# Optimization experiments

Measured on AMD Instinct MI355X. Metric: run time of the kernel, lower is better.

## Reference

```python
import jax, jax.numpy as jnp
import numpy as np

EPS = 1e-12  # torch F.normalize eps

def setup_inputs() -> dict:
    key = jax.random.key(0)
    ks = jax.random.split(key, 3)
    B, N, C, H, K = 4, 4096, 512, 8, 64
    x = jax.random.normal(ks[0], (B, N, C), dtype=jnp.float32)
    W_qkvv = jax.random.normal(ks[1], (4 * C, C), dtype=jnp.float32) * (1.0 / np.sqrt(C))
    # init_: uniform(-1/sqrt(K), 1/sqrt(K)) over [N, K]
    std = 1.0 / np.sqrt(K)
    EF = jax.random.uniform(ks[2], (N, K), dtype=jnp.float32, minval=-std, maxval=std)
    temperature = jnp.ones((H, 1, 1), dtype=jnp.float32)
    temperature2 = jnp.ones((H, 1, 1), dtype=jnp.float32)
    return {"x": x, "W_qkvv": W_qkvv, "EF": EF,
            "temperature": temperature, "temperature2": temperature2}

def _l2norm(t):
    # torch.nn.functional.normalize(dim=-1): x / max(||x||_2, eps)
    n = jnp.sqrt(jnp.sum(t * t, axis=-1, keepdims=True))
    return t / jnp.maximum(n, EPS)

def reference(x, W_qkvv, EF, temperature, temperature2):
    B, N, C = x.shape
    H = temperature.shape[0]
    d = C // H
    # fused QKVV projection (no bias)
    qkvv = (x @ W_qkvv.T).reshape(B, N, 4, H, d)
    qkvv = jnp.transpose(qkvv, (2, 0, 3, 1, 4))  # [4,B,H,N,d]
    # transpose last two dims -> [B,H,d,N]
    q = jnp.swapaxes(qkvv[0], -2, -1)
    k = jnp.swapaxes(qkvv[1], -2, -1)
    v_CA = jnp.swapaxes(qkvv[2], -2, -1)
    v_SA = jnp.swapaxes(qkvv[3], -2, -1)
    # Linformer-style EF projection over token axis: [B,H,d,N] x [N,K] -> [B,H,d,K]
    k_proj = jnp.einsum('bhdn,nk->bhdk', k, EF)
    v_proj = jnp.einsum('bhdn,nk->bhdk', v_SA, EF)
    # L2-normalize q,k over token axis
    qn = _l2norm(q)
    kn = _l2norm(k)
    # channel attention: [B,H,d,d]
    attn_CA = jax.nn.softmax(jnp.einsum('bhdn,bhen->bhde', qn, kn) * temperature, axis=-1)
    x_CA = jnp.einsum('bhde,bhen->bhdn', attn_CA, v_CA)           # [B,H,d,N]
    x_CA = jnp.transpose(x_CA, (0, 3, 1, 2)).reshape(B, N, C)      # [B,N,C]
    # spatial attention via projected K: [B,H,N,K]
    attn_SA = jax.nn.softmax(jnp.einsum('bhdn,bhdk->bhnk', qn, k_proj) * temperature2, axis=-1)
    x_SA = jnp.einsum('bhnk,bhdk->bhnd', attn_SA, v_proj)          # [B,H,N,d]
    # faithful to the original: permute(0,3,1,2) then reshape(B,N,C)
    x_SA = jnp.transpose(x_SA, (0, 3, 1, 2)).reshape(B, N, C)
    return x_CA + x_SA
```

## Files before the change

### kernel.cpp

```cpp
#include <hip/hip_runtime.h>

typedef unsigned short u16;
typedef unsigned int u32;
typedef __attribute__((ext_vector_type(8))) short s16x8;
typedef __attribute__((ext_vector_type(4))) float f32x4;

#define MFMA16(a,b,c) __builtin_amdgcn_mfma_f32_16x16x32_bf16(a,b,c,0,0,0)

__device__ __forceinline__ u16 f2bf(float f){
  u32 u = __builtin_bit_cast(u32, f);
  return (u16)((u + 0x7FFFu + ((u >> 16) & 1u)) >> 16);
}
__device__ __forceinline__ float b2f(u16 s){
  u32 u = ((u32)s) << 16;
  return __builtin_bit_cast(float, u);
}
__device__ __forceinline__ int sw64(int row, int col){
  return row * 64 + ((((col >> 3) ^ row) & 7) << 3) + (col & 7);
}
__device__ __forceinline__ void async16(const void* g, void* l){
  __builtin_amdgcn_global_load_lds((const __attribute__((address_space(1))) u32*)g,
                                   (__attribute__((address_space(3))) u32*)l, 16, 0, 0);
}


__global__ __launch_bounds__(256) void k_convert(const float4* __restrict__ x4,
                                                 const float4* __restrict__ w4,
                                                 const float* __restrict__ EF,
                                                 u16* __restrict__ Xb, u16* __restrict__ Wb,
                                                 u16* __restrict__ EFt){
  int i = blockIdx.x * 256 + threadIdx.x;
  if (i < 2097152){
    float4 v = x4[i];
    u32 lo = (u32)f2bf(v.x) | ((u32)f2bf(v.y) << 16);
    u32 hi = (u32)f2bf(v.z) | ((u32)f2bf(v.w) << 16);
    *(uint2*)(&Xb[(size_t)i*4]) = make_uint2(lo, hi);
  } else if (i < 2097152 + 262144){
    int j = i - 2097152;
    float4 v = w4[j];
    u32 lo = (u32)f2bf(v.x) | ((u32)f2bf(v.y) << 16);
    u32 hi = (u32)f2bf(v.z) | ((u32)f2bf(v.w) << 16);
    *(uint2*)(&Wb[(size_t)j*4]) = make_uint2(lo, hi);
  } else if (i < 2097152 + 262144 + 262144){
    int j = i - 2097152 - 262144;
    int kk = j >> 12, nn = j & 4095;
    EFt[(size_t)kk*4096 + nn] = f2bf(EF[(size_t)nn*64 + kk]);
  }
}

__global__ __launch_bounds__(256) void k_gemm(const u16* __restrict__ Wb,
                                              const u16* __restrict__ Xb,
                                              u16* __restrict__ Out){
  __shared__ u16 smA[128*32];
  __shared__ u16 smB[128*32];
  int bid = blockIdx.x;
  int ot = bid & 15, mt = bid >> 4;
  int o0 = ot * 128, m0 = mt * 128;
  int t = threadIdx.x;
  int lane = t & 63, w = t >> 6;
  int wr = w >> 1, wc = w & 1;
  int l15 = lane & 15, l4 = lane >> 4;
  f32x4 acc[4][4];
#pragma unroll
  for (int a = 0; a < 4; ++a)
#pragma unroll
    for (int b = 0; b < 4; ++b) acc[a][b] = (f32x4){0.f, 0.f, 0.f, 0.f};

  for (int kt = 0; kt < 16; ++kt){
    int kb = kt * 32;
#pragma unroll
    for (int i = 0; i < 2; ++i){
      int la = t + 256 * i;
      async16(Wb + (size_t)(o0 + (la >> 2)) * 512 + kb + (la & 3) * 8, &smA[la * 8]);
      async16(Xb + (size_t)(m0 + (la >> 2)) * 512 + kb + (la & 3) * 8, &smB[la * 8]);
    }
    __syncthreads();
    s16x8 af[4], bfr[4];
#pragma unroll
    for (int rf = 0; rf < 4; ++rf) af[rf] = *(const s16x8*)(&smA[(wr*64 + rf*16 + l15)*32 + l4*8]);
#pragma unroll
    for (int cf = 0; cf < 4; ++cf) bfr[cf] = *(const s16x8*)(&smB[(wc*64 + cf*16 + l15)*32 + l4*8]);
#pragma unroll
    for (int rf = 0; rf < 4; ++rf)
#pragma unroll
      for (int cf = 0; cf < 4; ++cf)
        acc[rf][cf] = MFMA16(af[rf], bfr[cf], acc[rf][cf]);
    __syncthreads();
  }
#pragma unroll
  for (int rf = 0; rf < 4; ++rf)
#pragma unroll
    for (int cf = 0; cf < 4; ++cf){
      int o = o0 + wr*64 + rf*16 + l4*4;
      int m = m0 + wc*64 + cf*16 + l15;
#pragma unroll
      for (int r = 0; r < 4; ++r) Out[(size_t)(o + r) * 16384 + m] = f2bf(acc[rf][cf][r]);
    }
}

__global__ __launch_bounds__(64) void k_rnorm(const u16* __restrict__ QK,
                                              float* __restrict__ rq, float* __restrict__ rk){
  int bid = blockIdx.x;
  int o = bid >> 2, b = bid & 3;
  int lane = threadIdx.x;
  const u16* row = QK + (size_t)o * 16384 + (size_t)b * 4096;
  float s = 0.f;
#pragma unroll
  for (int it = 0; it < 8; ++it){
    s16x8 v = *(const s16x8*)(&row[it * 512 + lane * 8]);
#pragma unroll
    for (int j = 0; j < 8; ++j){ float f = b2f((u16)v[j]); s += f * f; }
  }
  for (int off = 32; off; off >>= 1) s += __shfl_down(s, off);
  if (lane == 0){
    float r = 1.f / fmaxf(sqrtf(s), 1e-12f);
    if (o < 512) rq[b * 512 + o] = r;
    else         rk[b * 512 + (o - 512)] = r;
  }
}

__global__ __launch_bounds__(256) void k_acc1(const u16* __restrict__ QK,
                                              const u16* __restrict__ EFt,
                                              float* __restrict__ Pp){
  int bid = blockIdx.x;
  int p = bid >> 8;
  int rem = bid & 255;
  int bh = rem >> 3, s = rem & 7;
  int b = bh >> 3, h = bh & 7;
  int t = threadIdx.x, lane = t & 63, w = t >> 6, l15 = lane & 15, l4 = lane >> 4;
  int abase = (p == 0 ? 0 : (p == 1 ? 512 : 1536)) + h * 64;
  const u16* aptr = QK + (size_t)(abase + w*16 + l15) * 16384 + (size_t)b * 4096 + s * 512;
  f32x4 acc[4];
#pragma unroll
  for (int c = 0; c < 4; ++c) acc[c] = (f32x4){0.f,0.f,0.f,0.f};

  if (p == 0){
    const u16* bptr = QK + (size_t)(512 + h*64 + l15) * 16384 + (size_t)b * 4096 + s * 512;
#pragma unroll 2
    for (int ks = 0; ks < 16; ++ks){
      int n = ks * 32 + l4 * 8;
      s16x8 a = *(const s16x8*)(aptr + n);
#pragma unroll
      for (int cf = 0; cf < 4; ++cf){
        s16x8 bb = *(const s16x8*)(bptr + (size_t)cf * 16 * 16384 + n);
        acc[cf] = MFMA16(a, bb, acc[cf]);
      }
    }
  } else {
    const u16* bptr = EFt + (size_t)l15 * 4096 + s * 512;
#pragma unroll 2
    for (int ks = 0; ks < 16; ++ks){
      int n = ks * 32 + l4 * 8;
      s16x8 a = *(const s16x8*)(aptr + n);
#pragma unroll
      for (int cf = 0; cf < 4; ++cf){
        s16x8 bb = *(const s16x8*)(bptr + (size_t)cf * 16 * 4096 + n);
        acc[cf] = MFMA16(a, bb, acc[cf]);
      }
    }
  }

  float* out = Pp + ((size_t)(bh * 3 + p) * 8 + s) * 4096;
#pragma unroll
  for (int cf = 0; cf < 4; ++cf)
#pragma unroll
    for (int r = 0; r < 4; ++r){
      int rr = w*16 + l4*4 + r;
      int cc = cf*16 + l15;
      int off = (p == 1) ? (cc * 64 + rr) : (rr * 64 + cc);
      out[off] = acc[cf][r];
    }
}

__global__ __launch_bounds__(256) void k_fin(const float* __restrict__ Pp,
                                             const float* __restrict__ rq,
                                             const float* __restrict__ rk,
                                             const float* __restrict__ t1,
                                             const float* __restrict__ t2,
                                             u16* __restrict__ Pca,
                                             u16* __restrict__ kpb,
                                             u16* __restrict__ vpb){
  int bh = blockIdx.x;
  int b = bh >> 3, h = bh & 7;
  int t = threadIdx.x;
  int row = t >> 2, q4 = t & 3;
  const float* base = Pp + (size_t)bh * 3 * 8 * 4096;
  float t1h = t1[h], t2h = t2[h];
  const float* rqh = rq + b*512 + h*64;
  const float* rkh = rk + b*512 + h*64;

  {
    float v[16];
#pragma unroll
    for (int i = 0; i < 4; ++i){
      f32x4 a = (f32x4){0.f,0.f,0.f,0.f};
#pragma unroll
      for (int s = 0; s < 8; ++s)
        a += *(const f32x4*)(base + (size_t)s * 4096 + t*16 + i*4);
#pragma unroll
      for (int j = 0; j < 4; ++j) v[i*4 + j] = a[j];
    }
    float sq = rqh[row] * t1h;
#pragma unroll
    for (int e = 0; e < 16; ++e) v[e] *= sq * rkh[q4*16 + e];
    float mx = v[0];
#pragma unroll
    for (int e = 1; e < 16; ++e) mx = fmaxf(mx, v[e]);
    mx = fmaxf(mx, __shfl_xor(mx, 1));
    mx = fmaxf(mx, __shfl_xor(mx, 2));
    float sum = 0.f;
#pragma unroll
    for (int e = 0; e < 16; ++e){ v[e] = __expf(v[e] - mx); sum += v[e]; }
    sum += __shfl_xor(sum, 1);
    sum += __shfl_xor(sum, 2);
    float inv = 1.f / sum;
    s16x8 o0, o1;
#pragma unroll
    for (int e = 0; e < 8; ++e){ o0[e] = (short)f2bf(v[e] * inv); o1[e] = (short)f2bf(v[8+e] * inv); }
    *(s16x8*)(&Pca[(size_t)bh*4096 + t*16])     = o0;
    *(s16x8*)(&Pca[(size_t)bh*4096 + t*16 + 8]) = o1;
  }
  {
    const float* p1 = base + 8 * 4096;
    float v[16];
#pragma unroll
    for (int i = 0; i < 4; ++i){
      f32x4 a = (f32x4){0.f,0.f,0.f,0.f};
#pragma unroll
      for (int s = 0; s < 8; ++s)
        a += *(const f32x4*)(p1 + (size_t)s * 4096 + t*16 + i*4);
#pragma unroll
      for (int j = 0; j < 4; ++j) v[i*4 + j] = a[j];
    }
    s16x8 o0, o1;
#pragma unroll
    for (int e = 0; e < 8; ++e){
      o0[e] = (short)f2bf(v[e]   * rqh[q4*16 + e]     * t2h);
      o1[e] = (short)f2bf(v[8+e] * rqh[q4*16 + 8 + e] * t2h);
    }
    *(s16x8*)(&kpb[(size_t)bh*4096 + t*16])     = o0;
    *(s16x8*)(&kpb[(size_t)bh*4096 + t*16 + 8]) = o1;
  }
  {
    const float* p2 = base + 16 * 4096;
    float v[16];
#pragma unroll
    for (int i = 0; i < 4; ++i){
      f32x4 a = (f32x4){0.f,0.f,0.f,0.f};
#pragma unroll
      for (int s = 0; s < 8; ++s)
        a += *(const f32x4*)(p2 + (size_t)s * 4096 + t*16 + i*4);
#pragma unroll
      for (int j = 0; j < 4; ++j) v[i*4 + j] = a[j];
    }
    s16x8 o0, o1;
#pragma unroll
    for (int e = 0; e < 8; ++e){ o0[e] = (short)f2bf(v[e]); o1[e] = (short)f2bf(v[8+e]); }
    *(s16x8*)(&vpb[(size_t)bh*4096 + t*16])     = o0;
    *(s16x8*)(&vpb[(size_t)bh*4096 + t*16 + 8]) = o1;
  }
}

__global__ __launch_bounds__(256) void k_ca_pv(const u16* __restrict__ QK,
                                               const u16* __restrict__ Pca,
                                               float* __restrict__ out){
  __shared__ u16 Pl[64*64];
  __shared__ u16 Vt[64*64];
  __shared__ float Sx[64*64];
  int bid = blockIdx.x;
  int ch = bid & 63, bh = bid >> 6, b = bh >> 3, h = bh & 7;
  int n0 = ch * 64;
  int t = threadIdx.x, lane = t & 63, w = t >> 6, l15 = lane & 15, l4 = lane >> 4;
#pragma unroll
  for (int i = 0; i < 16; ++i){
    int idx = t + 256 * i;
    Pl[sw64(idx >> 6, idx & 63)] = Pca[(size_t)bh * 4096 + idx];
    int e = idx >> 6, j = idx & 63;
    Vt[sw64(j, e)] = QK[(size_t)(1024 + h*64 + e) * 16384 + (size_t)b*4096 + n0 + j];
  }
  __syncthreads();
  f32x4 acc[4];
#pragma unroll
  for (int c = 0; c < 4; ++c) acc[c] = (f32x4){0.f,0.f,0.f,0.f};
#pragma unroll
  for (int ks = 0; ks < 2; ++ks){
    s16x8 a = *(const s16x8*)(&Pl[sw64(w*16 + l15, ks*32 + l4*8)]);
#pragma unroll
    for (int cf = 0; cf < 4; ++cf){
      s16x8 bb = *(const s16x8*)(&Vt[sw64(cf*16 + l15, ks*32 + l4*8)]);
      acc[cf] = MFMA16(a, bb, acc[cf]);
    }
  }
#pragma unroll
  for (int cf = 0; cf < 4; ++cf)
#pragma unroll
    for (int r = 0; r < 4; ++r){
      int d = w*16 + l4*4 + r, j = cf*16 + l15;
      Sx[j*64 + d] = acc[cf][r];
    }
  __syncthreads();
#pragma unroll
  for (int i = 0; i < 4; ++i){
    int idx = t + 256 * i;
    int j = idx >> 4, v = idx & 15;
    float4 val;
    val.x = Sx[j*64 + v*4 + 0]; val.y = Sx[j*64 + v*4 + 1];
    val.z = Sx[j*64 + v*4 + 2]; val.w = Sx[j*64 + v*4 + 3];
    *(float4*)(&out[((size_t)(b*4096 + n0 + j)) * 512 + h*64 + v*4]) = val;
  }
}

__global__ __launch_bounds__(256) void k_sa(const u16* __restrict__ QK,
                                            const u16* __restrict__ kpb,
                                            const u16* __restrict__ vpb,
                                            float* __restrict__ out){
  __shared__ u16 Qt[64*64];
  __shared__ float Sf[64*64];
  __shared__ u16 kpl[64*64];
  __shared__ u16 vpl[64*64];
  int bid = blockIdx.x;
  int ch = bid & 63, bh = bid >> 6, b = bh >> 3, h = bh & 7;
  int n0 = ch * 64;
  int t = threadIdx.x, lane = t & 63, w = t >> 6, l15 = lane & 15, l4 = lane >> 4;
#pragma unroll
  for (int i = 0; i < 16; ++i){
    int idx = t + 256 * i;
    int row = idx >> 6, col = idx & 63;
    kpl[sw64(row, col)] = kpb[(size_t)bh * 4096 + idx];
    vpl[sw64(row, col)] = vpb[(size_t)bh * 4096 + idx];
    int dd = row, j = col;
    Qt[sw64(j, dd)] = QK[(size_t)(h*64 + dd) * 16384 + (size_t)b*4096 + n0 + j];
  }
  __syncthreads();
  f32x4 acc[4];
#pragma unroll
  for (int c = 0; c < 4; ++c) acc[c] = (f32x4){0.f,0.f,0.f,0.f};
#pragma unroll
  for (int ks = 0; ks < 2; ++ks){
    s16x8 a = *(const s16x8*)(&Qt[sw64(w*16 + l15, ks*32 + l4*8)]);
#pragma unroll
    for (int cf = 0; cf < 4; ++cf){
      s16x8 bb = *(const s16x8*)(&kpl[sw64(cf*16 + l15, ks*32 + l4*8)]);
      acc[cf] = MFMA16(a, bb, acc[cf]);
    }
  }
#pragma unroll
  for (int cf = 0; cf < 4; ++cf)
#pragma unroll
    for (int r = 0; r < 4; ++r){
      int j = w*16 + l4*4 + r, kk = cf*16 + l15;
      Sf[j*64 + kk] = acc[cf][r];
    }
  __syncthreads();
  if (t < 64){
    float mx = -1e30f;
    for (int it = 0; it < 64; ++it){ int kk = (t + it) & 63; mx = fmaxf(mx, Sf[t*64 + kk]); }
    float sum = 0.f;
    for (int it = 0; it < 64; ++it){ int kk = (t + it) & 63; sum += __expf(Sf[t*64 + kk] - mx); }
    float inv = 1.f / sum;
    for (int it = 0; it < 64; ++it){
      int kk = (t + it) & 63;
      Qt[sw64(t, kk)] = f2bf(__expf(Sf[t*64 + kk] - mx) * inv);
    }
  }
  __syncthreads();
  f32x4 acc2[4];
#pragma unroll
  for (int c = 0; c < 4; ++c) acc2[c] = (f32x4){0.f,0.f,0.f,0.f};
#pragma unroll
  for (int ks = 0; ks < 2; ++ks){
    s16x8 a = *(const s16x8*)(&Qt[sw64(w*16 + l15, ks*32 + l4*8)]);
#pragma unroll
    for (int cf = 0; cf < 4; ++cf){
      s16x8 bb = *(const s16x8*)(&vpl[sw64(cf*16 + l15, ks*32 + l4*8)]);
      acc2[cf] = MFMA16(a, bb, acc2[cf]);
    }
  }
#pragma unroll
  for (int cf = 0; cf < 4; ++cf)
#pragma unroll
    for (int r = 0; r < 4; ++r){
      int j = w*16 + l4*4 + r, dd = cf*16 + l15;
      Sf[dd*64 + j] = acc2[cf][r];
    }
  __syncthreads();
#pragma unroll
  for (int i = 0; i < 4; ++i){
    int idx = t + 256 * i;
    int dd = idx >> 4, v = idx & 15;
    size_t p = (size_t)b*2097152 + (size_t)dd*32768 + (size_t)h*4096 + n0 + v*4;
    float4 cur = *(float4*)(&out[p]);
    cur.x += Sf[dd*64 + v*4 + 0]; cur.y += Sf[dd*64 + v*4 + 1];
    cur.z += Sf[dd*64 + v*4 + 2]; cur.w += Sf[dd*64 + v*4 + 3];
    *(float4*)(&out[p]) = cur;
  }
}

extern "C" void kernel_launch(void* const* d_in, const int* in_sizes, int n_in,
                              void* d_out, int out_size, void* d_ws, size_t ws_size,
                              hipStream_t stream) {
  const float* x  = (const float*)d_in[0];
  const float* Wq = (const float*)d_in[1];
  const float* EF = (const float*)d_in[2];
  const float* t1 = (const float*)d_in[3];
  const float* t2 = (const float*)d_in[4];
  float* out = (float*)d_out;

  u16* Xb  = (u16*)d_ws;
  u16* Wb  = Xb + 8388608;
  u16* EFt = Wb + 1048576;
  u16* QK  = EFt + 262144;
  float* rq  = (float*)(QK + 33554432);
  float* rk  = rq + 2048;
  u16* kpb = (u16*)(rk + 2048);
  u16* vpb = kpb + 131072;
  u16* Pca = vpb + 131072;
  float* Pp = (float*)d_ws;

  k_convert<<<10240, 256, 0, stream>>>((const float4*)x, (const float4*)Wq, EF, Xb, Wb, EFt);
  k_gemm   <<<2048, 256, 0, stream>>>(Wb, Xb, QK);
  k_rnorm  <<<4096, 64, 0, stream>>>(QK, rq, rk);
  k_acc1   <<<768,  256, 0, stream>>>(QK, EFt, Pp);
  k_fin    <<<32,   256, 0, stream>>>(Pp, rq, rk, t1, t2, Pca, kpb, vpb);
  k_ca_pv  <<<2048, 256, 0, stream>>>(QK, Pca, out);
  k_sa     <<<2048, 256, 0, stream>>>(QK, kpb, vpb, out);
}
```

Before: 221.6 us.

## Swizzle LDS layouts, stage acc1 via LDS, softmax in registers, remap GEMM blocks

Several independent changes. The GEMM gets an XOR swizzle on its LDS tiles and a block-index remap, and k_rnorm packs four rows per 256-thread block. k_acc1 now stages its operands through double-buffered LDS with async global-to-LDS loads. k_fin writes its small matrices pre-swizzled so k_ca_pv and k_sa can copy them with async16 and do a vectorised transpose of Q/V. k_sa computes the softmax in registers with shuffles instead of using a single-wave pass over LDS; these aim to cut bank conflicts, scalar global loads and serial softmax work, at the cost of more complex indexing and manual waitcnt/barrier handling.

After: 198.6 us. 10.4% less time.

```diff
diff --git a/kernel.cpp b/kernel.cpp
--- a/kernel.cpp
+++ b/kernel.cpp
@@ -14,9 +14,6 @@
 __device__ __forceinline__ float b2f(u16 s){
   u32 u = ((u32)s) << 16;
   return __builtin_bit_cast(float, u);
-}
-__device__ __forceinline__ int sw64(int row, int col){
-  return row * 64 + ((((col >> 3) ^ row) & 7) << 3) + (col & 7);
 }
 __device__ __forceinline__ void async16(const void* g, void* l){
   __builtin_amdgcn_global_load_lds((const __attribute__((address_space(1))) u32*)g,
@@ -54,7 +51,8 @@
   __shared__ u16 smA[128*32];
   __shared__ u16 smB[128*32];
   int bid = blockIdx.x;
-  int ot = bid & 15, mt = bid >> 4;
+  int sbid = (bid & 7) * 256 + (bid >> 3);
+  int ot = sbid & 15, mt = sbid >> 4;
   int o0 = ot * 128, m0 = mt * 128;
   int t = threadIdx.x;
   int lane = t & 63, w = t >> 6;
@@ -71,15 +69,23 @@
 #pragma unroll
     for (int i = 0; i < 2; ++i){
       int la = t + 256 * i;
-      async16(Wb + (size_t)(o0 + (la >> 2)) * 512 + kb + (la & 3) * 8, &smA[la * 8]);
-      async16(Xb + (size_t)(m0 + (la >> 2)) * 512 + kb + (la & 3) * 8, &smB[la * 8]);
+      int row = la >> 2, sl = la & 3;
+      int sg = sl ^ ((row >> 1) & 3);
+      async16(Wb + (size_t)(o0 + row) * 512 + kb + sg * 8, &smA[la * 8]);
+      async16(Xb + (size_t)(m0 + row) * 512 + kb + sg * 8, &smB[la * 8]);
     }
     __syncthreads();
     s16x8 af[4], bfr[4];
 #pragma unroll
-    for (int rf = 0; rf < 4; ++rf) af[rf] = *(const s16x8*)(&smA[(wr*64 + rf*16 + l15)*32 + l4*8]);
-#pragma unroll
-    for (int cf = 0; cf < 4; ++cf) bfr[cf] = *(const s16x8*)(&smB[(wc*64 + cf*16 + l15)*32 + l4*8]);
+    for (int rf = 0; rf < 4; ++rf){
+      int row = wr*64 + rf*16 + l15;
+      af[rf] = *(const s16x8*)(&smA[row*32 + ((l4 ^ ((row >> 1) & 3)))*8]);
+    }
+#pragma unroll
+    for (int cf = 0; cf < 4; ++cf){
+      int row = wc*64 + cf*16 + l15;
+      bfr[cf] = *(const s16x8*)(&smB[row*32 + ((l4 ^ ((row >> 1) & 3)))*8]);
+    }
 #pragma unroll
     for (int rf = 0; rf < 4; ++rf)
 #pragma unroll
@@ -98,11 +104,11 @@
     }
 }
 
-__global__ __launch_bounds__(64) void k_rnorm(const u16* __restrict__ QK,
-                                              float* __restrict__ rq, float* __restrict__ rk){
-  int bid = blockIdx.x;
-  int o = bid >> 2, b = bid & 3;
-  int lane = threadIdx.x;
+__global__ __launch_bounds__(256) void k_rnorm(const u16* __restrict__ QK,
+                                               float* __restrict__ rq, float* __restrict__ rk){
+  int job = blockIdx.x * 4 + (threadIdx.x >> 6);
+  int o = job >> 2, b = job & 3;
+  int lane = threadIdx.x & 63;
   const u16* row = QK + (size_t)o * 16384 + (size_t)b * 4096;
   float s = 0.f;
 #pragma unroll
@@ -122,6 +128,8 @@
 __global__ __launch_bounds__(256) void k_acc1(const u16* __restrict__ QK,
                                               const u16* __restrict__ EFt,
                                               float* __restrict__ Pp){
+  __shared__ u16 Ab[2][64*128];
+  __shared__ u16 Bb[2][64*128];
   int bid = blockIdx.x;
   int p = bid >> 8;
   int rem = bid & 255;
@@ -129,35 +137,59 @@
   int b = bh >> 3, h = bh & 7;
   int t = threadIdx.x, lane = t & 63, w = t >> 6, l15 = lane & 15, l4 = lane >> 4;
   int abase = (p == 0 ? 0 : (p == 1 ? 512 : 1536)) + h * 64;
-  const u16* aptr = QK + (size_t)(abase + w*16 + l15) * 16384 + (size_t)b * 4096 + s * 512;
+  const u16* Aglob = QK + (size_t)abase * 16384 + (size_t)b * 4096 + s * 512;
+  const u16* Bglob;
+  size_t bstride;
+  if (p == 0){ Bglob = QK + (size_t)(512 + h*64) * 16384 + (size_t)b * 4096 + s * 512; bstride = 16384; }
+  else       { Bglob = EFt + s * 512; bstride = 4096; }
+  int srow = t >> 4, sslot = t & 15;
+
+#define STAGE_ACC(ch, buf)                                                        \
+  {                                                                               \
+    int n0_ = (ch) * 128;                                                         \
+    _Pragma("unroll")                                                             \
+    for (int c = 0; c < 4; ++c){                                                  \
+      int row = c*16 + srow;                                                      \
+      int sg = sslot ^ (row & 7);                                                 \
+      async16(Aglob + (size_t)row * 16384 + n0_ + sg*8, &Ab[buf][row*128 + sslot*8]); \
+    }                                                                             \
+    _Pragma("unroll")                                                             \
+    for (int c = 0; c < 4; ++c){                                                  \
+      int row = c*16 + srow;                                                      \
+      int sg = sslot ^ (row & 7);                                                 \
+      async16(Bglob + (size_t)row * bstride + n0_ + sg*8, &Bb[buf][row*128 + sslot*8]); \
+    }                                                                             \
+  }
+
   f32x4 acc[4];
 #pragma unroll
   for (int c = 0; c < 4; ++c) acc[c] = (f32x4){0.f,0.f,0.f,0.f};
 
-  if (p == 0){
-    const u16* bptr = QK + (size_t)(512 + h*64 + l15) * 16384 + (size_t)b * 4096 + s * 512;
-#pragma unroll 2
-    for (int ks = 0; ks < 16; ++ks){
-      int n = ks * 32 + l4 * 8;
-      s16x8 a = *(const s16x8*)(aptr + n);
+  STAGE_ACC(0, 0);
+#pragma unroll
+  for (int ch = 0; ch < 4; ++ch){
+    int buf = ch & 1;
+    if (ch < 3){
+      STAGE_ACC(ch + 1, buf ^ 1);
+      asm volatile("s_waitcnt vmcnt(8)" ::: "memory");
+    } else {
+      asm volatile("s_waitcnt vmcnt(0)" ::: "memory");
+    }
+    __builtin_amdgcn_s_barrier();
+    asm volatile("" ::: "memory");
+    int arow = w*16 + l15;
+#pragma unroll
+    for (int ks = 0; ks < 4; ++ks){
+      s16x8 a = *(const s16x8*)(&Ab[buf][arow*128 + (((ks*4 + l4) ^ (arow & 7)))*8]);
 #pragma unroll
       for (int cf = 0; cf < 4; ++cf){
-        s16x8 bb = *(const s16x8*)(bptr + (size_t)cf * 16 * 16384 + n);
+        int brow = cf*16 + l15;
+        s16x8 bb = *(const s16x8*)(&Bb[buf][brow*128 + (((ks*4 + l4) ^ (brow & 7)))*8]);
         acc[cf] = MFMA16(a, bb, acc[cf]);
       }
     }
-  } else {
-    const u16* bptr = EFt + (size_t)l15 * 4096 + s * 512;
-#pragma unroll 2
-    for (int ks = 0; ks < 16; ++ks){
-      int n = ks * 32 + l4 * 8;
-      s16x8 a = *(const s16x8*)(aptr + n);
-#pragma unroll
-      for (int cf = 0; cf < 4; ++cf){
-        s16x8 bb = *(const s16x8*)(bptr + (size_t)cf * 16 * 4096 + n);
-        acc[cf] = MFMA16(a, bb, acc[cf]);
-      }
-    }
+    __builtin_amdgcn_s_barrier();
+    asm volatile("" ::: "memory");
   }
 
   float* out = Pp + ((size_t)(bh * 3 + p) * 8 + s) * 4096;
@@ -170,6 +202,7 @@
       int off = (p == 1) ? (cc * 64 + rr) : (rr * 64 + cc);
       out[off] = acc[cf][r];
     }
+#undef STAGE_ACC
 }
 
 __global__ __launch_bounds__(256) void k_fin(const float* __restrict__ Pp,
@@ -188,6 +221,8 @@
   float t1h = t1[h], t2h = t2[h];
   const float* rqh = rq + b*512 + h*64;
   const float* rkh = rk + b*512 + h*64;
+  int sA = (((q4*2)     ^ (row & 7)) << 3);
+  int sB = (((q4*2 + 1) ^ (row & 7)) << 3);
 
   {
     float v[16];
@@ -217,8 +252,8 @@
     s16x8 o0, o1;
 #pragma unroll
     for (int e = 0; e < 8; ++e){ o0[e] = (short)f2bf(v[e] * inv); o1[e] = (short)f2bf(v[8+e] * inv); }
-    *(s16x8*)(&Pca[(size_t)bh*4096 + t*16])     = o0;
-    *(s16x8*)(&Pca[(size_t)bh*4096 + t*16 + 8]) = o1;
+    *(s16x8*)(&Pca[(size_t)bh*4096 + row*64 + sA]) = o0;
+    *(s16x8*)(&Pca[(size_t)bh*4096 + row*64 + sB]) = o1;
   }
   {
     const float* p1 = base + 8 * 4096;
@@ -238,8 +273,8 @@
       o0[e] = (short)f2bf(v[e]   * rqh[q4*16 + e]     * t2h);
       o1[e] = (short)f2bf(v[8+e] * rqh[q4*16 + 8 + e] * t2h);
     }
-    *(s16x8*)(&kpb[(size_t)bh*4096 + t*16])     = o0;
-    *(s16x8*)(&kpb[(size_t)bh*4096 + t*16 + 8]) = o1;
+    *(s16x8*)(&kpb[(size_t)bh*4096 + row*64 + sA]) = o0;
+    *(s16x8*)(&kpb[(size_t)bh*4096 + row*64 + sB]) = o1;
   }
   {
     const float* p2 = base + 16 * 4096;
@@ -256,8 +291,8 @@
     s16x8 o0, o1;
 #pragma unroll
     for (int e = 0; e < 8; ++e){ o0[e] = (short)f2bf(v[e]); o1[e] = (short)f2bf(v[8+e]); }
-    *(s16x8*)(&vpb[(size_t)bh*4096 + t*16])     = o0;
-    *(s16x8*)(&vpb[(size_t)bh*4096 + t*16 + 8]) = o1;
+    *(s16x8*)(&vpb[(size_t)bh*4096 + row*64 + sA]) = o0;
+    *(s16x8*)(&vpb[(size_t)bh*4096 + row*64 + sB]) = o1;
   }
 }
 
@@ -271,23 +306,36 @@
   int ch = bid & 63, bh = bid >> 6, b = bh >> 3, h = bh & 7;
   int n0 = ch * 64;
   int t = threadIdx.x, lane = t & 63, w = t >> 6, l15 = lane & 15, l4 = lane >> 4;
-#pragma unroll
-  for (int i = 0; i < 16; ++i){
-    int idx = t + 256 * i;
-    Pl[sw64(idx >> 6, idx & 63)] = Pca[(size_t)bh * 4096 + idx];
-    int e = idx >> 6, j = idx & 63;
-    Vt[sw64(j, e)] = QK[(size_t)(1024 + h*64 + e) * 16384 + (size_t)b*4096 + n0 + j];
+  {
+    const u16* src = Pca + (size_t)bh * 4096;
+#pragma unroll
+    for (int c = 0; c < 2; ++c)
+      async16(src + (c*256 + t)*8, &Pl[(c*256 + t)*8]);
+  }
+  const u16* Vg = QK + (size_t)(1024 + h*64) * 16384 + (size_t)b*4096 + n0;
+#pragma unroll
+  for (int pass = 0; pass < 2; ++pass){
+    int idx = pass*256 + t;
+    int e = idx >> 3, j0 = (idx & 7) * 8;
+    s16x8 v = *(const s16x8*)(Vg + (size_t)e * 16384 + j0);
+#pragma unroll
+    for (int i = 0; i < 8; ++i){
+      int j = j0 + i;
+      Vt[j*64 + ((((e>>3) ^ (j & 7))) << 3) + (e & 7)] = (u16)v[i];
+    }
   }
   __syncthreads();
   f32x4 acc[4];
 #pragma unroll
   for (int c = 0; c < 4; ++c) acc[c] = (f32x4){0.f,0.f,0.f,0.f};
+  int ar = w*16 + l15;
 #pragma unroll
   for (int ks = 0; ks < 2; ++ks){
-    s16x8 a = *(const s16x8*)(&Pl[sw64(w*16 + l15, ks*32 + l4*8)]);
+    s16x8 a = *(const s16x8*)(&Pl[ar*64 + (((ks*4 + l4) ^ (ar & 7)))*8]);
 #pragma unroll
     for (int cf = 0; cf < 4; ++cf){
-      s16x8 bb = *(const s16x8*)(&Vt[sw64(cf*16 + l15, ks*32 + l4*8)]);
+      int br = cf*16 + l15;
+      s16x8 bb = *(const s16x8*)(&Vt[br*64 + (((ks*4 + l4) ^ (br & 7)))*8]);
       acc[cf] = MFMA16(a, bb, acc[cf]);
     }
   }
@@ -315,64 +363,82 @@
                                             const u16* __restrict__ vpb,
                                             float* __restrict__ out){
   __shared__ u16 Qt[64*64];
-  __shared__ float Sf[64*64];
   __shared__ u16 kpl[64*64];
   __shared__ u16 vpl[64*64];
+  __shared__ float Sf[64*64];
   int bid = blockIdx.x;
   int ch = bid & 63, bh = bid >> 6, b = bh >> 3, h = bh & 7;
   int n0 = ch * 64;
   int t = threadIdx.x, lane = t & 63, w = t >> 6, l15 = lane & 15, l4 = lane >> 4;
 #pragma unroll
-  for (int i = 0; i < 16; ++i){
-    int idx = t + 256 * i;
-    int row = idx >> 6, col = idx & 63;
-    kpl[sw64(row, col)] = kpb[(size_t)bh * 4096 + idx];
-    vpl[sw64(row, col)] = vpb[(size_t)bh * 4096 + idx];
-    int dd = row, j = col;
-    Qt[sw64(j, dd)] = QK[(size_t)(h*64 + dd) * 16384 + (size_t)b*4096 + n0 + j];
+  for (int c = 0; c < 2; ++c){
+    async16(kpb + (size_t)bh*4096 + (c*256 + t)*8, &kpl[(c*256 + t)*8]);
+    async16(vpb + (size_t)bh*4096 + (c*256 + t)*8, &vpl[(c*256 + t)*8]);
+  }
+  const u16* Qg = QK + (size_t)(h*64) * 16384 + (size_t)b*4096 + n0;
+#pragma unroll
+  for (int pass = 0; pass < 2; ++pass){
+    int idx = pass*256 + t;
+    int dd = idx >> 3, j0 = (idx & 7) * 8;
+    s16x8 v = *(const s16x8*)(Qg + (size_t)dd * 16384 + j0);
+#pragma unroll
+    for (int i = 0; i < 8; ++i){
+      int j = j0 + i;
+      Qt[j*64 + ((((dd>>3) ^ (j & 7))) << 3) + (dd & 7)] = (u16)v[i];
+    }
   }
   __syncthreads();
   f32x4 acc[4];
 #pragma unroll
   for (int c = 0; c < 4; ++c) acc[c] = (f32x4){0.f,0.f,0.f,0.f};
+  int ar = w*16 + l15;
 #pragma unroll
   for (int ks = 0; ks < 2; ++ks){
-    s16x8 a = *(const s16x8*)(&Qt[sw64(w*16 + l15, ks*32 + l4*8)]);
+    s16x8 a = *(const s16x8*)(&Qt[ar*64 + (((ks*4 + l4) ^ (ar & 7)))*8]);
 #pragma unroll
     for (int cf = 0; cf < 4; ++cf){
-      s16x8 bb = *(const s16x8*)(&kpl[sw64(cf*16 + l15, ks*32 + l4*8)]);
+      int br = cf*16 + l15;
+      s16x8 bb = *(const s16x8*)(&kpl[br*64 + (((ks*4 + l4) ^ (br & 7)))*8]);
       acc[cf] = MFMA16(a, bb, acc[cf]);
     }
   }
 #pragma unroll
+  for (int r = 0; r < 4; ++r){
+    float mx = fmaxf(fmaxf(acc[0][r], acc[1][r]), fmaxf(acc[2][r], acc[3][r]));
+    mx = fmaxf(mx, __shfl_xor(mx, 1));
+    mx = fmaxf(mx, __shfl_xor(mx, 2));
+    mx = fmaxf(mx, __shfl_xor(mx, 4));
+    mx = fmaxf(mx, __shfl_xor(mx, 8));
+    float sum = 0.f;
+#pragma unroll
+    for (int cf = 0; cf < 4; ++cf){ acc[cf][r] = __expf(acc[cf][r] - mx); sum += acc[cf][r]; }
+    sum += __shfl_xor(sum, 1);
+    sum += __shfl_xor(sum, 2);
+    sum += __shfl_xor(sum, 4);
+    sum += __shfl_xor(sum, 8);
+    float inv = 1.f / sum;
+#pragma unroll
+    for (int cf = 0; cf < 4; ++cf) acc[cf][r] *= inv;
+  }
+#pragma unroll
   for (int cf = 0; cf < 4; ++cf)
 #pragma unroll
     for (int r = 0; r < 4; ++r){
-      int j = w*16 + l4*4 + r, kk = cf*16 + l15;
-      Sf[j*64 + kk] = acc[cf][r];
-    }
-  __syncthreads();
-  if (t < 64){
-    float mx = -1e30f;
-    for (int it = 0; it < 64; ++it){ int kk = (t + it) & 63; mx = fmaxf(mx, Sf[t*64 + kk]); }
-    float sum = 0.f;
-    for (int it = 0; it < 64; ++it){ int kk = (t + it) & 63; sum += __expf(Sf[t*64 + kk] - mx); }
-    float inv = 1.f / sum;
-    for (int it = 0; it < 64; ++it){
-      int kk = (t + it) & 63;
-      Qt[sw64(t, kk)] = f2bf(__expf(Sf[t*64 + kk] - mx) * inv);
-    }
-  }
+      int j = w*16 + l4*4 + r;
+      int kslot = cf*2 + (l15 >> 3);
+      Qt[j*64 + ((kslot ^ (j & 7)) << 3) + (l15 & 7)] = f2bf(acc[cf][r]);
+    }
   __syncthreads();
   f32x4 acc2[4];
 #pragma unroll
   for (int c = 0; c < 4; ++c) acc2[c] = (f32x4){0.f,0.f,0.f,0.f};
 #pragma unroll
   for (int ks = 0; ks < 2; ++ks){
-    s16x8 a = *(const s16x8*)(&Qt[sw64(w*16 + l15, ks*32 + l4*8)]);
+    s16x8 a = *(const s16x8*)(&Qt[ar*64 + (((ks*4 + l4) ^ (ar & 7)))*8]);
 #pragma unroll
     for (int cf = 0; cf < 4; ++cf){
-      s16x8 bb = *(const s16x8*)(&vpl[sw64(cf*16 + l15, ks*32 + l4*8)]);
+      int br = cf*16 + l15;
+      s16x8 bb = *(const s16x8*)(&vpl[br*64 + (((ks*4 + l4) ^ (br & 7)))*8]);
       acc2[cf] = MFMA16(a, bb, acc2[cf]);
     }
   }
@@ -419,7 +485,7 @@
 
   k_convert<<<10240, 256, 0, stream>>>((const float4*)x, (const float4*)Wq, EF, Xb, Wb, EFt);
   k_gemm   <<<2048, 256, 0, stream>>>(Wb, Xb, QK);
-  k_rnorm  <<<4096, 64, 0, stream>>>(QK, rq, rk);
+  k_rnorm  <<<1024, 256, 0, stream>>>(QK, rq, rk);
   k_acc1   <<<768,  256, 0, stream>>>(QK, EFt, Pp);
   k_fin    <<<32,   256, 0, stream>>>(Pp, rq, rk, t1, t2, Pca, kpb, vpb);
   k_ca_pv  <<<2048, 256, 0, stream>>>(QK, Pca, out);
```
